# Kernel tuning notes

Measured on AMD Instinct MI355X. Metric: run time of the kernel, lower is better.

Reference implementation:

```python
import jax, jax.numpy as jnp
import numpy as np

NUM_EXPERTS = 32
TOP_K = 4
HIDDEN = 2048
INTER = 768


def setup_inputs() -> dict:
    key = jax.random.key(0)
    k1, k2, k3, k4 = jax.random.split(key, 4)
    hidden_states = jax.random.normal(k1, (4, 512, HIDDEN), dtype=jnp.float32)
    gate = jax.random.normal(k2, (HIDDEN, NUM_EXPERTS), dtype=jnp.float32) * 0.02
    gate_up_proj = jax.random.normal(k3, (NUM_EXPERTS, HIDDEN, 2 * INTER), dtype=jnp.float32) * 0.02
    down_proj = jax.random.normal(k4, (NUM_EXPERTS, INTER, HIDDEN), dtype=jnp.float32) * 0.02
    return {"hidden_states": hidden_states, "gate": gate,
            "gate_up_proj": gate_up_proj, "down_proj": down_proj}


def reference(hidden_states, gate, gate_up_proj, down_proj):
    batch_size = hidden_states.shape[0]
    x = hidden_states.reshape(-1, HIDDEN)  # (T, D)
    num_tokens = x.shape[0]

    # Router
    router_logits = jnp.einsum('TD,DE->TE', x, gate)
    routing_weights = jax.nn.softmax(router_logits.astype(jnp.float32), axis=-1)
    top_k_weights, top_k_indices = jax.lax.top_k(routing_weights, TOP_K)
    top_k_weights = top_k_weights / top_k_weights.sum(axis=-1, keepdims=True)
    top_k_weights = top_k_weights.astype(x.dtype)

    # Scatter top-k weights into full (T, E) matrix
    router_weights = jnp.zeros((num_tokens, NUM_EXPERTS), dtype=x.dtype)
    token_indices = jnp.broadcast_to(jnp.arange(num_tokens)[:, None], top_k_indices.shape)
    router_weights = router_weights.at[token_indices, top_k_indices].set(top_k_weights)

    # Dense all-expert experts pass (faithful to original: computes every expert per token)
    gate_up = jnp.einsum('TD,EDF->TEF', x, gate_up_proj)  # (T, E, 2F)
    g, u = jnp.split(gate_up, 2, axis=-1)
    gated = u * jax.nn.silu(g)  # (T, E, F)
    next_states = jnp.einsum('TEF,EFD->TED', gated, down_proj)
    next_states = (next_states * router_weights[..., None]).sum(axis=1)  # (T, D)
    return next_states.reshape(batch_size, -1, HIDDEN)
```

## Files before the change

kernel.cpp:

```cpp
#include <hip/hip_runtime.h>

#define T_TOKENS 2048
#define HIDDEN   2048
#define NEXPERT  32
#define TOPK     4
#define INTER    768
#define NPAIRS   (T_TOKENS*TOPK)
#define BM       128
#define BK       32
#define MT_MAX   95
#define NT1      12
#define NT2      16
#define NK1      (HIDDEN/BK)
#define NK2      (INTER/BK)

typedef short  bh8 __attribute__((ext_vector_type(8)));
typedef float  fx4 __attribute__((ext_vector_type(4)));

#define AS1 __attribute__((address_space(1)))
#define AS3 __attribute__((address_space(3)))

__device__ __forceinline__ void gload_lds16(const void* g, const void* lds_generic){
    __builtin_amdgcn_global_load_lds(
        (const AS1 void*)(unsigned long long)g,
        (AS3 void*)(unsigned int)(unsigned long long)lds_generic,
        16, 0, 0);
}

__device__ __forceinline__ unsigned int pack2bf(float a, float b){
    unsigned ua = __float_as_uint(a) + 0x8000u;
    unsigned ub = __float_as_uint(b) + 0x8000u;
    return __builtin_amdgcn_perm(ub, ua, 0x07060302u);
}
__device__ __forceinline__ unsigned short f2bfu(float f){
    return (unsigned short)((__float_as_uint(f) + 0x8000u) >> 16);
}

__global__ void cvt_x_k(const float* __restrict__ x, unsigned short* __restrict__ xb){
    int i = (blockIdx.x*256 + threadIdx.x)*8;
    float4 a = *(const float4*)(x+i);
    float4 b = *(const float4*)(x+i+4);
    uint4 o;
    o.x = pack2bf(a.x,a.y); o.y = pack2bf(a.z,a.w);
    o.z = pack2bf(b.x,b.y); o.w = pack2bf(b.z,b.w);
    *(uint4*)(xb+i) = o;
}

__global__ void router_k(const float* __restrict__ x, const float* __restrict__ gate,
                         int* __restrict__ topk_id, float* __restrict__ topk_w,
                         int* __restrict__ counts){
    const int t = blockIdx.x;
    const int l = threadIdx.x;
    const float* xr = x + (size_t)t*HIDDEN;
    float acc[NEXPERT];
#pragma unroll
    for (int e=0;e<NEXPERT;e++) acc[e]=0.f;
    for (int d=l; d<HIDDEN; d+=64){
        float xv = xr[d];
        const float4* g4 = (const float4*)(gate + (size_t)d*NEXPERT);
#pragma unroll
        for (int i=0;i<8;i++){
            float4 g = g4[i];
            acc[i*4+0] += xv*g.x; acc[i*4+1] += xv*g.y;
            acc[i*4+2] += xv*g.z; acc[i*4+3] += xv*g.w;
        }
    }
#pragma unroll
    for (int e=0;e<NEXPERT;e++){
#pragma unroll
        for (int m=1;m<64;m<<=1) acc[e] += __shfl_xor(acc[e], m, 64);
    }
    int ids[TOPK]; float lv[TOPK];
#pragma unroll
    for (int k=0;k<TOPK;k++){
        float m=-1e30f; int mi=0;
#pragma unroll
        for (int e=0;e<NEXPERT;e++){ if (acc[e]>m){ m=acc[e]; mi=e; } }
        ids[k]=mi; lv[k]=m; acc[mi]=-1e30f;
    }
    float ex[TOPK]; float s=0.f;
#pragma unroll
    for (int k=0;k<TOPK;k++){ ex[k]=__expf(lv[k]-lv[0]); s+=ex[k]; }
    if (l==0){
        float inv = 1.f/s;
#pragma unroll
        for (int k=0;k<TOPK;k++){
            topk_id[t*TOPK+k]=ids[k];
            topk_w[t*TOPK+k]=ex[k]*inv;
            atomicAdd(&counts[ids[k]],1);
        }
    }
}

__global__ void sched_k(const int* __restrict__ counts, int* __restrict__ offs,
                        int* __restrict__ cursors, int* __restrict__ nmt,
                        int* __restrict__ te, int* __restrict__ tr0, int* __restrict__ trn){
    if (threadIdx.x==0 && blockIdx.x==0){
        int tot=0, nm=0;
        for (int e=0;e<NEXPERT;e++){
            int c = counts[e];
            offs[e]=tot; cursors[e]=tot;
            for (int s=0;s<c;s+=BM){
                te[nm]=e; tr0[nm]=tot+s; trn[nm]=(c-s)<BM?(c-s):BM; nm++;
            }
            tot+=c;
        }
        *nmt = nm;
    }
}

__global__ void scatter_k(const int* __restrict__ topk_id, const float* __restrict__ topk_w,
                          int* __restrict__ cursors, int* __restrict__ pair_tok,
                          float* __restrict__ pair_w){
    int g = blockIdx.x*256 + threadIdx.x;
    int e = topk_id[g];
    float w = topk_w[g];
    int pos = atomicAdd(&cursors[e],1);
    pair_tok[pos] = g>>2;
    pair_w[pos]  = w;
}

__global__ __launch_bounds__(256) void gemm1_k(
        const unsigned short* __restrict__ xb, const float* __restrict__ gup,
        const int* __restrict__ nmt, const int* __restrict__ te,
        const int* __restrict__ tr0, const int* __restrict__ trn,
        const int* __restrict__ pair_tok, const float* __restrict__ pair_w,
        unsigned short* __restrict__ gated){
    __shared__ __align__(16) unsigned short As[2][BM*32];
    __shared__ __align__(16) unsigned short Bs[BM*40];
    __shared__ int   s_tok[BM];
    __shared__ float s_w[BM];

    const int nwg = gridDim.x;
    const int q = nwg>>3, r = nwg&7;
    const int xcd = blockIdx.x & 7, bidx = blockIdx.x >> 3;
    const int L = (xcd<r ? xcd*(q+1) : r*(q+1)+(xcd-r)*q) + bidx;
    const int mt = L % MT_MAX, nt = L / MT_MAX;
    if (mt >= *nmt) return;
    const int e = te[mt], row0 = tr0[mt], rows = trn[mt];
    const int n0 = nt*64;

    const int t = threadIdx.x;
    if (t < BM){
        int p = row0 + t; if (p > NPAIRS-1) p = NPAIRS-1;
        s_tok[t] = pair_tok[p];
        s_w[t]   = pair_w[p];
    }
    __syncthreads();

    const int w = t>>6, lane = t&63;
    const int l15 = lane & 15, kb = lane >> 4;

    const int arow0 = w*16 + (lane>>2);
    const int arow1 = 64 + arow0;
    const int ck0 = (lane&3) ^ ((lane>>3)&3);
    const unsigned short* asrc0 = xb + (size_t)s_tok[arow0]*HIDDEN + ck0*8;
    const unsigned short* asrc1 = xb + (size_t)s_tok[arow1]*HIDDEN + ck0*8;
    const unsigned short* adst0[2] = { &As[0][(w*16)*32],      &As[1][(w*16)*32] };
    const unsigned short* adst1[2] = { &As[0][(64+w*16)*32],   &As[1][(64+w*16)*32] };

    const int j5 = t & 31, col4 = j5*4;
    const int bd0 = (t>>5)*4;
    const int gq = (j5>>1)&3;
    const unsigned wb = (unsigned)(col4*80 + (((bd0>>3) ^ gq)<<4) + (bd0&4)*2);
    const int fc = (col4 < 64) ? (n0 + col4) : (704 + n0 + col4);
    const float* bsrc = gup + (size_t)e*HIDDEN*(2*INTER) + (size_t)bd0*(2*INTER) + fc;

    fx4 acc[2][8];
#pragma unroll
    for (int i=0;i<2;i++)
#pragma unroll
        for (int j=0;j<8;j++) acc[i][j] = (fx4)0.f;

    gload_lds16(asrc0, adst0[0]);
    gload_lds16(asrc1, adst1[0]);
    float4 rv0 = *(const float4*)(bsrc);
    float4 rv1 = *(const float4*)(bsrc + 2*INTER);
    float4 rv2 = *(const float4*)(bsrc + 4*INTER);
    float4 rv3 = *(const float4*)(bsrc + 6*INTER);

    const int sA = (l15>>1)&3;
    char* bsb = (char*)Bs;
    for (int k=0; k<NK1; ++k){
        __syncthreads();
        *(uint2*)(bsb + wb      ) = make_uint2(pack2bf(rv0.x,rv1.x), pack2bf(rv2.x,rv3.x));
        *(uint2*)(bsb + wb +  80) = make_uint2(pack2bf(rv0.y,rv1.y), pack2bf(rv2.y,rv3.y));
        *(uint2*)(bsb + wb + 160) = make_uint2(pack2bf(rv0.z,rv1.z), pack2bf(rv2.z,rv3.z));
        *(uint2*)(bsb + wb + 240) = make_uint2(pack2bf(rv0.w,rv1.w), pack2bf(rv2.w,rv3.w));
        __syncthreads();
        if (k+1 < NK1){
            const float* b2 = bsrc + (size_t)(k+1)*BK*(2*INTER);
            rv0 = *(const float4*)(b2);
            rv1 = *(const float4*)(b2 + 2*INTER);
            rv2 = *(const float4*)(b2 + 4*INTER);
            rv3 = *(const float4*)(b2 + 6*INTER);
            gload_lds16(asrc0 + (k+1)*BK, adst0[(k+1)&1]);
            gload_lds16(asrc1 + (k+1)*BK, adst1[(k+1)&1]);
        }
        const unsigned short* Ak = As[k&1];
        bh8 a0 = *(const bh8*)(Ak + (w*32+l15)*32    + ((kb ^ sA)<<3));
        bh8 a1 = *(const bh8*)(Ak + (w*32+16+l15)*32 + ((kb ^ sA)<<3));
#pragma unroll
        for (int c=0;c<8;c++){
            const int bc = c*16 + l15;
            bh8 b = *(const bh8*)(bsb + bc*80 + ((kb ^ ((bc>>3)&3))<<4));
            acc[0][c] = __builtin_amdgcn_mfma_f32_16x16x32_bf16(a0, b, acc[0][c], 0,0,0);
            acc[1][c] = __builtin_amdgcn_mfma_f32_16x16x32_bf16(a1, b, acc[1][c], 0,0,0);
        }
    }

    const int rbase = w*32 + kb*4;
#pragma unroll
    for (int mr=0;mr<2;mr++){
#pragma unroll
        for (int qq=0;qq<4;qq++){
            int row = rbase + mr*16 + qq;
            if (row < rows){
                float wgt = s_w[row];
                size_t prow = (size_t)(row0 + row)*INTER + n0 + l15;
#pragma unroll
                for (int c=0;c<4;c++){
                    float g = acc[mr][c][qq], u = acc[mr][c+4][qq];
                    float sil = g / (1.f + __expf(-g));
                    gated[prow + c*16] = f2bfu(sil*u*wgt);
                }
            }
        }
    }
}

__global__ __launch_bounds__(256) void gemm2_k(
        const unsigned short* __restrict__ gated, const float* __restrict__ down,
        const int* __restrict__ nmt, const int* __restrict__ te,
        const int* __restrict__ tr0, const int* __restrict__ trn,
        const int* __restrict__ pair_tok, float* __restrict__ out){
    __shared__ __align__(16) unsigned short As[2][BM*32];
    __shared__ __align__(16) unsigned short Bs[BM*40];
    __shared__ int s_tok[BM];

    const int nwg = gridDim.x;
    const int q = nwg>>3, r = nwg&7;
    const int xcd = blockIdx.x & 7, bidx = blockIdx.x >> 3;
    const int L = (xcd<r ? xcd*(q+1) : r*(q+1)+(xcd-r)*q) + bidx;
    const int mt = L % MT_MAX, nt = L / MT_MAX;
    if (mt >= *nmt) return;
    const int e = te[mt], row0 = tr0[mt], rows = trn[mt];
    const int n0 = nt*128;

    const int t = threadIdx.x;
    if (t < BM){
        int p = row0 + t; if (p > NPAIRS-1) p = NPAIRS-1;
        s_tok[t] = pair_tok[p];
    }
    __syncthreads();

    const int w = t>>6, lane = t&63;
    const int l15 = lane & 15, kb = lane >> 4;

    const int arow0 = w*16 + (lane>>2);
    const int arow1 = 64 + arow0;
    const int ck0 = (lane&3) ^ ((lane>>3)&3);
    const unsigned short* asrc0 = gated + (size_t)(row0 + arow0)*INTER + ck0*8;
    const unsigned short* asrc1 = gated + (size_t)(row0 + arow1)*INTER + ck0*8;
    const unsigned short* adst0[2] = { &As[0][(w*16)*32],    &As[1][(w*16)*32] };
    const unsigned short* adst1[2] = { &As[0][(64+w*16)*32], &As[1][(64+w*16)*32] };

    const int j5 = t & 31, col4 = j5*4;
    const int bd0 = (t>>5)*4;
    const int gq = (j5>>1)&3;
    const unsigned wb = (unsigned)(col4*80 + (((bd0>>3) ^ gq)<<4) + (bd0&4)*2);
    const float* bsrc = down + (size_t)e*INTER*HIDDEN + (size_t)bd0*HIDDEN + (n0 + col4);

    fx4 acc[2][8];
#pragma unroll
    for (int i=0;i<2;i++)
#pragma unroll
        for (int j=0;j<8;j++) acc[i][j] = (fx4)0.f;

    gload_lds16(asrc0, adst0[0]);
    gload_lds16(asrc1, adst1[0]);
    float4 rv0 = *(const float4*)(bsrc);
    float4 rv1 = *(const float4*)(bsrc + HIDDEN);
    float4 rv2 = *(const float4*)(bsrc + 2*HIDDEN);
    float4 rv3 = *(const float4*)(bsrc + 3*HIDDEN);

    const int sA = (l15>>1)&3;
    char* bsb = (char*)Bs;
    for (int k=0; k<NK2; ++k){
        __syncthreads();
        *(uint2*)(bsb + wb      ) = make_uint2(pack2bf(rv0.x,rv1.x), pack2bf(rv2.x,rv3.x));
        *(uint2*)(bsb + wb +  80) = make_uint2(pack2bf(rv0.y,rv1.y), pack2bf(rv2.y,rv3.y));
        *(uint2*)(bsb + wb + 160) = make_uint2(pack2bf(rv0.z,rv1.z), pack2bf(rv2.z,rv3.z));
        *(uint2*)(bsb + wb + 240) = make_uint2(pack2bf(rv0.w,rv1.w), pack2bf(rv2.w,rv3.w));
        __syncthreads();
        if (k+1 < NK2){
            const float* b2 = bsrc + (size_t)(k+1)*BK*HIDDEN;
            rv0 = *(const float4*)(b2);
            rv1 = *(const float4*)(b2 + HIDDEN);
            rv2 = *(const float4*)(b2 + 2*HIDDEN);
            rv3 = *(const float4*)(b2 + 3*HIDDEN);
            gload_lds16(asrc0 + (k+1)*BK, adst0[(k+1)&1]);
            gload_lds16(asrc1 + (k+1)*BK, adst1[(k+1)&1]);
        }
        const unsigned short* Ak = As[k&1];
        bh8 a0 = *(const bh8*)(Ak + (w*32+l15)*32    + ((kb ^ sA)<<3));
        bh8 a1 = *(const bh8*)(Ak + (w*32+16+l15)*32 + ((kb ^ sA)<<3));
#pragma unroll
        for (int c=0;c<8;c++){
            const int bc = c*16 + l15;
            bh8 b = *(const bh8*)(bsb + bc*80 + ((kb ^ ((bc>>3)&3))<<4));
            acc[0][c] = __builtin_amdgcn_mfma_f32_16x16x32_bf16(a0, b, acc[0][c], 0,0,0);
            acc[1][c] = __builtin_amdgcn_mfma_f32_16x16x32_bf16(a1, b, acc[1][c], 0,0,0);
        }
    }

    const int rbase = w*32 + kb*4;
#pragma unroll
    for (int mr=0;mr<2;mr++){
#pragma unroll
        for (int qq=0;qq<4;qq++){
            int row = rbase + mr*16 + qq;
            if (row < rows){
                float* orow = out + (size_t)s_tok[row]*HIDDEN + n0 + l15;
#pragma unroll
                for (int c=0;c<8;c++)
                    atomicAdd(orow + c*16, acc[mr][c][qq]);
            }
        }
    }
}

extern "C" void kernel_launch(void* const* d_in, const int* in_sizes, int n_in,
                              void* d_out, int out_size, void* d_ws, size_t ws_size,
                              hipStream_t stream){
    const float* x    = (const float*)d_in[0];
    const float* gate = (const float*)d_in[1];
    const float* gup  = (const float*)d_in[2];
    const float* down = (const float*)d_in[3];
    float* out = (float*)d_out;
    char*  ws  = (char*)d_ws;

    int*   topk_id  = (int*)  (ws + 0x00000);
    float* topk_w   = (float*)(ws + 0x08000);
    int*   counts   = (int*)  (ws + 0x10000);
    int*   cursors  = (int*)  (ws + 0x10080);
    int*   offs     = (int*)  (ws + 0x10100);
    int*   nmt      = (int*)  (ws + 0x10180);
    int*   te       = (int*)  (ws + 0x10200);
    int*   tr0      = (int*)  (ws + 0x10400);
    int*   trn      = (int*)  (ws + 0x10600);
    int*   pair_tok = (int*)  (ws + 0x10800);
    float* pair_w   = (float*)(ws + 0x18800);
    unsigned short* gated = (unsigned short*)(ws + 0x21000);
    unsigned short* xb    = (unsigned short*)(ws + 0xC60000);

    hipMemsetAsync(d_out, 0, (size_t)out_size*sizeof(float), stream);
    hipMemsetAsync(counts, 0, NEXPERT*sizeof(int), stream);

    cvt_x_k  <<<T_TOKENS*HIDDEN/(256*8), 256, 0, stream>>>(x, xb);
    router_k <<<T_TOKENS, 64, 0, stream>>>(x, gate, topk_id, topk_w, counts);
    sched_k  <<<1, 64, 0, stream>>>(counts, offs, cursors, nmt, te, tr0, trn);
    scatter_k<<<NPAIRS/256, 256, 0, stream>>>(topk_id, topk_w, cursors, pair_tok, pair_w);
    gemm1_k  <<<MT_MAX*NT1, 256, 0, stream>>>(xb, gup, nmt, te, tr0, trn, pair_tok, pair_w, gated);
    gemm2_k  <<<MT_MAX*NT2, 256, 0, stream>>>(gated, down, nmt, te, tr0, trn, pair_tok, out);
}
```

Baseline: 429.0 us.

## Halve GEMM N-tiles and double-buffer B tile with single barrier per k-step

```diff
diff --git a/kernel.cpp b/kernel.cpp
--- a/kernel.cpp
+++ b/kernel.cpp
@@ -9,8 +9,8 @@
 #define BM       128
 #define BK       32
 #define MT_MAX   95
-#define NT1      12
-#define NT2      16
+#define NT1      24
+#define NT2      32
 #define NK1      (HIDDEN/BK)
 #define NK2      (INTER/BK)
 
@@ -120,6 +120,15 @@
     pair_w[pos]  = w;
 }
 
+#define TILE_DECODE(NT)                                            \
+    const int nwg = gridDim.x;                                     \
+    const int q = nwg>>3, r = nwg&7;                               \
+    const int xcd = blockIdx.x & 7, bidx = blockIdx.x >> 3;        \
+    const int L = (xcd<r ? xcd*(q+1) : r*(q+1)+(xcd-r)*q) + bidx;  \
+    const int mt = L % MT_MAX, nt = L / MT_MAX;                    \
+    if (mt >= *nmt) return;                                        \
+    const int e = te[mt], row0 = tr0[mt], rows = trn[mt];
+
 __global__ __launch_bounds__(256) void gemm1_k(
         const unsigned short* __restrict__ xb, const float* __restrict__ gup,
         const int* __restrict__ nmt, const int* __restrict__ te,
@@ -127,18 +136,12 @@
         const int* __restrict__ pair_tok, const float* __restrict__ pair_w,
         unsigned short* __restrict__ gated){
     __shared__ __align__(16) unsigned short As[2][BM*32];
-    __shared__ __align__(16) unsigned short Bs[BM*40];
+    __shared__ __align__(16) unsigned short Bs[2][64*40];
     __shared__ int   s_tok[BM];
     __shared__ float s_w[BM];
 
-    const int nwg = gridDim.x;
-    const int q = nwg>>3, r = nwg&7;
-    const int xcd = blockIdx.x & 7, bidx = blockIdx.x >> 3;
-    const int L = (xcd<r ? xcd*(q+1) : r*(q+1)+(xcd-r)*q) + bidx;
-    const int mt = L % MT_MAX, nt = L / MT_MAX;
-    if (mt >= *nmt) return;
-    const int e = te[mt], row0 = tr0[mt], rows = trn[mt];
-    const int n0 = nt*64;
+    TILE_DECODE(NT1)
+    const int n0 = nt*32;
 
     const int t = threadIdx.x;
     if (t < BM){
@@ -150,64 +153,77 @@
 
     const int w = t>>6, lane = t&63;
     const int l15 = lane & 15, kb = lane >> 4;
+    const int sA = (l15>>1)&3;
 
     const int arow0 = w*16 + (lane>>2);
     const int arow1 = 64 + arow0;
     const int ck0 = (lane&3) ^ ((lane>>3)&3);
     const unsigned short* asrc0 = xb + (size_t)s_tok[arow0]*HIDDEN + ck0*8;
     const unsigned short* asrc1 = xb + (size_t)s_tok[arow1]*HIDDEN + ck0*8;
-    const unsigned short* adst0[2] = { &As[0][(w*16)*32],      &As[1][(w*16)*32] };
-    const unsigned short* adst1[2] = { &As[0][(64+w*16)*32],   &As[1][(64+w*16)*32] };
-
-    const int j5 = t & 31, col4 = j5*4;
-    const int bd0 = (t>>5)*4;
-    const int gq = (j5>>1)&3;
-    const unsigned wb = (unsigned)(col4*80 + (((bd0>>3) ^ gq)<<4) + (bd0&4)*2);
-    const int fc = (col4 < 64) ? (n0 + col4) : (704 + n0 + col4);
+
+    const int col4 = (t&15)*4;
+    const int bd0  = (t>>4)*2;
+    const int sB   = (col4>>3)&3;
+    const unsigned wb = (unsigned)(col4*80 + (((bd0>>3) ^ sB)<<4) + (bd0&7)*2);
+    const int fc = (col4 < 32) ? (n0 + col4) : (736 + n0 + col4);
     const float* bsrc = gup + (size_t)e*HIDDEN*(2*INTER) + (size_t)bd0*(2*INTER) + fc;
 
-    fx4 acc[2][8];
+    fx4 acc[2][4];
 #pragma unroll
     for (int i=0;i<2;i++)
 #pragma unroll
-        for (int j=0;j<8;j++) acc[i][j] = (fx4)0.f;
-
-    gload_lds16(asrc0, adst0[0]);
-    gload_lds16(asrc1, adst1[0]);
+        for (int j=0;j<4;j++) acc[i][j] = (fx4)0.f;
+
     float4 rv0 = *(const float4*)(bsrc);
     float4 rv1 = *(const float4*)(bsrc + 2*INTER);
-    float4 rv2 = *(const float4*)(bsrc + 4*INTER);
-    float4 rv3 = *(const float4*)(bsrc + 6*INTER);
-
-    const int sA = (l15>>1)&3;
-    char* bsb = (char*)Bs;
-    for (int k=0; k<NK1; ++k){
-        __syncthreads();
-        *(uint2*)(bsb + wb      ) = make_uint2(pack2bf(rv0.x,rv1.x), pack2bf(rv2.x,rv3.x));
-        *(uint2*)(bsb + wb +  80) = make_uint2(pack2bf(rv0.y,rv1.y), pack2bf(rv2.y,rv3.y));
-        *(uint2*)(bsb + wb + 160) = make_uint2(pack2bf(rv0.z,rv1.z), pack2bf(rv2.z,rv3.z));
-        *(uint2*)(bsb + wb + 240) = make_uint2(pack2bf(rv0.w,rv1.w), pack2bf(rv2.w,rv3.w));
-        __syncthreads();
-        if (k+1 < NK1){
-            const float* b2 = bsrc + (size_t)(k+1)*BK*(2*INTER);
-            rv0 = *(const float4*)(b2);
-            rv1 = *(const float4*)(b2 + 2*INTER);
-            rv2 = *(const float4*)(b2 + 4*INTER);
-            rv3 = *(const float4*)(b2 + 6*INTER);
-            gload_lds16(asrc0 + (k+1)*BK, adst0[(k+1)&1]);
-            gload_lds16(asrc1 + (k+1)*BK, adst1[(k+1)&1]);
-        }
-        const unsigned short* Ak = As[k&1];
-        bh8 a0 = *(const bh8*)(Ak + (w*32+l15)*32    + ((kb ^ sA)<<3));
-        bh8 a1 = *(const bh8*)(Ak + (w*32+16+l15)*32 + ((kb ^ sA)<<3));
-#pragma unroll
-        for (int c=0;c<8;c++){
-            const int bc = c*16 + l15;
-            bh8 b = *(const bh8*)(bsb + bc*80 + ((kb ^ ((bc>>3)&3))<<4));
-            acc[0][c] = __builtin_amdgcn_mfma_f32_16x16x32_bf16(a0, b, acc[0][c], 0,0,0);
-            acc[1][c] = __builtin_amdgcn_mfma_f32_16x16x32_bf16(a1, b, acc[1][c], 0,0,0);
-        }
-    }
+    gload_lds16(asrc0, &As[0][(w*16)*32]);
+    gload_lds16(asrc1, &As[0][(64+w*16)*32]);
+    __syncthreads();
+    {
+        char* bw = (char*)Bs[0];
+        *(unsigned*)(bw + wb      ) = pack2bf(rv0.x, rv1.x);
+        *(unsigned*)(bw + wb +  80) = pack2bf(rv0.y, rv1.y);
+        *(unsigned*)(bw + wb + 160) = pack2bf(rv0.z, rv1.z);
+        *(unsigned*)(bw + wb + 240) = pack2bf(rv0.w, rv1.w);
+    }
+    __syncthreads();
+
+#define G1_STEP(KK, CUR, NXT) do{                                              \
+    const int _kn = (KK)+1;                                                    \
+    if (_kn < NK1){                                                            \
+        const float* _b2 = bsrc + (size_t)_kn*BK*(2*INTER);                    \
+        rv0 = *(const float4*)(_b2);                                           \
+        rv1 = *(const float4*)(_b2 + 2*INTER);                                 \
+        gload_lds16(asrc0 + _kn*BK, &As[NXT][(w*16)*32]);                      \
+        gload_lds16(asrc1 + _kn*BK, &As[NXT][(64+w*16)*32]);                   \
+    }                                                                          \
+    {   const unsigned short* _Ak = As[CUR];                                   \
+        const char* _Bk = (const char*)Bs[CUR];                                \
+        bh8 _a0 = *(const bh8*)(_Ak + (w*32+l15)*32    + ((kb ^ sA)<<3));      \
+        bh8 _a1 = *(const bh8*)(_Ak + (w*32+16+l15)*32 + ((kb ^ sA)<<3));      \
+        _Pragma("unroll")                                                      \
+        for (int c=0;c<4;c++){                                                 \
+            const int bc = c*16 + l15;                                         \
+            bh8 _b = *(const bh8*)(_Bk + bc*80 + ((kb ^ ((bc>>3)&3))<<4));     \
+            acc[0][c] = __builtin_amdgcn_mfma_f32_16x16x32_bf16(_a0,_b,acc[0][c],0,0,0); \
+            acc[1][c] = __builtin_amdgcn_mfma_f32_16x16x32_bf16(_a1,_b,acc[1][c],0,0,0); \
+        }                                                                      \
+    }                                                                          \
+    if (_kn < NK1){                                                            \
+        char* _bw = (char*)Bs[NXT];                                            \
+        *(unsigned*)(_bw + wb      ) = pack2bf(rv0.x, rv1.x);                  \
+        *(unsigned*)(_bw + wb +  80) = pack2bf(rv0.y, rv1.y);                  \
+        *(unsigned*)(_bw + wb + 160) = pack2bf(rv0.z, rv1.z);                  \
+        *(unsigned*)(_bw + wb + 240) = pack2bf(rv0.w, rv1.w);                  \
+    }                                                                          \
+    __syncthreads();                                                           \
+}while(0)
+
+    for (int k2=0; k2<NK1; k2+=2){
+        G1_STEP(k2,   0, 1);
+        G1_STEP(k2+1, 1, 0);
+    }
+#undef G1_STEP
 
     const int rbase = w*32 + kb*4;
 #pragma unroll
@@ -219,8 +235,8 @@
                 float wgt = s_w[row];
                 size_t prow = (size_t)(row0 + row)*INTER + n0 + l15;
 #pragma unroll
-                for (int c=0;c<4;c++){
-                    float g = acc[mr][c][qq], u = acc[mr][c+4][qq];
+                for (int c=0;c<2;c++){
+                    float g = acc[mr][c][qq], u = acc[mr][c+2][qq];
                     float sil = g / (1.f + __expf(-g));
                     gated[prow + c*16] = f2bfu(sil*u*wgt);
                 }
@@ -235,17 +251,11 @@
         const int* __restrict__ tr0, const int* __restrict__ trn,
         const int* __restrict__ pair_tok, float* __restrict__ out){
     __shared__ __align__(16) unsigned short As[2][BM*32];
-    __shared__ __align__(16) unsigned short Bs[BM*40];
+    __shared__ __align__(16) unsigned short Bs[2][64*40];
     __shared__ int s_tok[BM];
 
-    const int nwg = gridDim.x;
-    const int q = nwg>>3, r = nwg&7;
-    const int xcd = blockIdx.x & 7, bidx = blockIdx.x >> 3;
-    const int L = (xcd<r ? xcd*(q+1) : r*(q+1)+(xcd-r)*q) + bidx;
-    const int mt = L % MT_MAX, nt = L / MT_MAX;
-    if (mt >= *nmt) return;
-    const int e = te[mt], row0 = tr0[mt], rows = trn[mt];
-    const int n0 = nt*128;
+    TILE_DECODE(NT2)
+    const int n0 = nt*64;
 
     const int t = threadIdx.x;
     if (t < BM){
@@ -256,63 +266,78 @@
 
     const int w = t>>6, lane = t&63;
     const int l15 = lane & 15, kb = lane >> 4;
+    const int sA = (l15>>1)&3;
 
     const int arow0 = w*16 + (lane>>2);
     const int arow1 = 64 + arow0;
     const int ck0 = (lane&3) ^ ((lane>>3)&3);
-    const unsigned short* asrc0 = gated + (size_t)(row0 + arow0)*INTER + ck0*8;
-    const unsigned short* asrc1 = gated + (size_t)(row0 + arow1)*INTER + ck0*8;
-    const unsigned short* adst0[2] = { &As[0][(w*16)*32],    &As[1][(w*16)*32] };
-    const unsigned short* adst1[2] = { &As[0][(64+w*16)*32], &As[1][(64+w*16)*32] };
-
-    const int j5 = t & 31, col4 = j5*4;
-    const int bd0 = (t>>5)*4;
-    const int gq = (j5>>1)&3;
-    const unsigned wb = (unsigned)(col4*80 + (((bd0>>3) ^ gq)<<4) + (bd0&4)*2);
+    int ap0 = row0 + arow0; if (ap0 > NPAIRS-1) ap0 = NPAIRS-1;
+    int ap1 = row0 + arow1; if (ap1 > NPAIRS-1) ap1 = NPAIRS-1;
+    const unsigned short* asrc0 = gated + (size_t)ap0*INTER + ck0*8;
+    const unsigned short* asrc1 = gated + (size_t)ap1*INTER + ck0*8;
+
+    const int col4 = (t&15)*4;
+    const int bd0  = (t>>4)*2;
+    const int sB   = (col4>>3)&3;
+    const unsigned wb = (unsigned)(col4*80 + (((bd0>>3) ^ sB)<<4) + (bd0&7)*2);
     const float* bsrc = down + (size_t)e*INTER*HIDDEN + (size_t)bd0*HIDDEN + (n0 + col4);
 
-    fx4 acc[2][8];
+    fx4 acc[2][4];
 #pragma unroll
     for (int i=0;i<2;i++)
 #pragma unroll
-        for (int j=0;j<8;j++) acc[i][j] = (fx4)0.f;
-
-    gload_lds16(asrc0, adst0[0]);
-    gload_lds16(asrc1, adst1[0]);
+        for (int j=0;j<4;j++) acc[i][j] = (fx4)0.f;
+
     float4 rv0 = *(const float4*)(bsrc);
     float4 rv1 = *(const float4*)(bsrc + HIDDEN);
-    float4 rv2 = *(const float4*)(bsrc + 2*HIDDEN);
-    float4 rv3 = *(const float4*)(bsrc + 3*HIDDEN);
-
-    const int sA = (l15>>1)&3;
-    char* bsb = (char*)Bs;
-    for (int k=0; k<NK2; ++k){
-        __syncthreads();
-        *(uint2*)(bsb + wb      ) = make_uint2(pack2bf(rv0.x,rv1.x), pack2bf(rv2.x,rv3.x));
-        *(uint2*)(bsb + wb +  80) = make_uint2(pack2bf(rv0.y,rv1.y), pack2bf(rv2.y,rv3.y));
-        *(uint2*)(bsb + wb + 160) = make_uint2(pack2bf(rv0.z,rv1.z), pack2bf(rv2.z,rv3.z));
-        *(uint2*)(bsb + wb + 240) = make_uint2(pack2bf(rv0.w,rv1.w), pack2bf(rv2.w,rv3.w));
-        __syncthreads();
-        if (k+1 < NK2){
-            const float* b2 = bsrc + (size_t)(k+1)*BK*HIDDEN;
-            rv0 = *(const float4*)(b2);
-            rv1 = *(const float4*)(b2 + HIDDEN);
-            rv2 = *(const float4*)(b2 + 2*HIDDEN);
-            rv3 = *(const float4*)(b2 + 3*HIDDEN);
-            gload_lds16(asrc0 + (k+1)*BK, adst0[(k+1)&1]);
-            gload_lds16(asrc1 + (k+1)*BK, adst1[(k+1)&1]);
-        }
-        const unsigned short* Ak = As[k&1];
-        bh8 a0 = *(const bh8*)(Ak + (w*32+l15)*32    + ((kb ^ sA)<<3));
-        bh8 a1 = *(const bh8*)(Ak + (w*32+16+l15)*32 + ((kb ^ sA)<<3));
-#pragma unroll
-        for (int c=0;c<8;c++){
-            const int bc = c*16 + l15;
-            bh8 b = *(const bh8*)(bsb + bc*80 + ((kb ^ ((bc>>3)&3))<<4));
-            acc[0][c] = __builtin_amdgcn_mfma_f32_16x16x32_bf16(a0, b, acc[0][c], 0,0,0);
-            acc[1][c] = __builtin_amdgcn_mfma_f32_16x16x32_bf16(a1, b, acc[1][c], 0,0,0);
-        }
-    }
+    gload_lds16(asrc0, &As[0][(w*16)*32]);
+    gload_lds16(asrc1, &As[0][(64+w*16)*32]);
+    __syncthreads();
+    {
+        char* bw = (char*)Bs[0];
+        *(unsigned*)(bw + wb      ) = pack2bf(rv0.x, rv1.x);
+        *(unsigned*)(bw + wb +  80) = pack2bf(rv0.y, rv1.y);
+        *(unsigned*)(bw + wb + 160) = pack2bf(rv0.z, rv1.z);
+        *(unsigned*)(bw + wb + 240) = pack2bf(rv0.w, rv1.w);
+    }
+    __syncthreads();
+
+#define G2_STEP(KK, CUR, NXT) do{                                              \
+    const int _kn = (KK)+1;                                                    \
+    if (_kn < NK2){                                                            \
+        const float* _b2 = bsrc + (size_t)_kn*BK*HIDDEN;                       \
+        rv0 = *(const float4*)(_b2);                                           \
+        rv1 = *(const float4*)(_b2 + HIDDEN);                                  \
+        gload_lds16(asrc0 + _kn*BK, &As[NXT][(w*16)*32]);                      \
+        gload_lds16(asrc1 + _kn*BK, &As[NXT][(64+w*16)*32]);                   \
+    }                                                                          \
+    {   const unsigned short* _Ak = As[CUR];                                   \
+        const char* _Bk = (const char*)Bs[CUR];                                \
+        bh8 _a0 = *(const bh8*)(_Ak + (w*32+l15)*32    + ((kb ^ sA)<<3));      \
+        bh8 _a1 = *(const bh8*)(_Ak + (w*32+16+l15)*32 + ((kb ^ sA)<<3));      \
+        _Pragma("unroll")                                                      \
+        for (int c=0;c<4;c++){                                                 \
+            const int bc = c*16 + l15;                                         \
+            bh8 _b = *(const bh8*)(_Bk + bc*80 + ((kb ^ ((bc>>3)&3))<<4));     \
+            acc[0][c] = __builtin_amdgcn_mfma_f32_16x16x32_bf16(_a0,_b,acc[0][c],0,0,0); \
+            acc[1][c] = __builtin_amdgcn_mfma_f32_16x16x32_bf16(_a1,_b,acc[1][c],0,0,0); \
+        }                                                                      \
+    }                                                                          \
+    if (_kn < NK2){                                                            \
+        char* _bw = (char*)Bs[NXT];                                            \
+        *(unsigned*)(_bw + wb      ) = pack2bf(rv0.x, rv1.x);                  \
+        *(unsigned*)(_bw + wb +  80) = pack2bf(rv0.y, rv1.y);                  \
+        *(unsigned*)(_bw + wb + 160) = pack2bf(rv0.z, rv1.z);                  \
+        *(unsigned*)(_bw + wb + 240) = pack2bf(rv0.w, rv1.w);                  \
+    }                                                                          \
+    __syncthreads();                                                           \
+}while(0)
+
+    for (int k2=0; k2<NK2; k2+=2){
+        G2_STEP(k2,   0, 1);
+        G2_STEP(k2+1, 1, 0);
+    }
+#undef G2_STEP
 
     const int rbase = w*32 + kb*4;
 #pragma unroll
@@ -323,7 +348,7 @@
             if (row < rows){
                 float* orow = out + (size_t)s_tok[row]*HIDDEN + n0 + l15;
 #pragma unroll
-                for (int c=0;c<8;c++)
+                for (int c=0;c<4;c++)
                     atomicAdd(orow + c*16, acc[mr][c][qq]);
             }
         }
```

Result: slower. 471.6 us (+9.9%).

## Widen GEMM N-tiles to 256 with 512-thread blocks and double-buffered B

Applied to the files above, without the earlier changes.

```diff
diff --git a/kernel.cpp b/kernel.cpp
--- a/kernel.cpp
+++ b/kernel.cpp
@@ -5,12 +5,13 @@
 #define NEXPERT  32
 #define TOPK     4
 #define INTER    768
+#define GUF      (2*INTER)
 #define NPAIRS   (T_TOKENS*TOPK)
 #define BM       128
 #define BK       32
 #define MT_MAX   95
-#define NT1      12
-#define NT2      16
+#define NT1      6
+#define NT2      8
 #define NK1      (HIDDEN/BK)
 #define NK2      (INTER/BK)
 
@@ -34,6 +35,9 @@
 }
 __device__ __forceinline__ unsigned short f2bfu(float f){
     return (unsigned short)((__float_as_uint(f) + 0x8000u) >> 16);
+}
+__device__ __forceinline__ float bf2f(unsigned short s){
+    return __uint_as_float(((unsigned)s)<<16);
 }
 
 __global__ void cvt_x_k(const float* __restrict__ x, unsigned short* __restrict__ xb){
@@ -120,51 +124,47 @@
     pair_w[pos]  = w;
 }
 
-__global__ __launch_bounds__(256) void gemm1_k(
+#define TILE_DECODE()                                              \
+    const int nwg = gridDim.x;                                     \
+    const int q = nwg>>3, r = nwg&7;                               \
+    const int xcd = blockIdx.x & 7, bidx = blockIdx.x >> 3;        \
+    const int L = (xcd<r ? xcd*(q+1) : r*(q+1)+(xcd-r)*q) + bidx;  \
+    const int mt = L % MT_MAX, nt = L / MT_MAX;                    \
+    if (mt >= *nmt) return;                                        \
+    const int e = te[mt], row0 = tr0[mt], rows = trn[mt];
+
+__global__ __launch_bounds__(512,4) void gemm1_k(
         const unsigned short* __restrict__ xb, const float* __restrict__ gup,
         const int* __restrict__ nmt, const int* __restrict__ te,
         const int* __restrict__ tr0, const int* __restrict__ trn,
-        const int* __restrict__ pair_tok, const float* __restrict__ pair_w,
-        unsigned short* __restrict__ gated){
+        const int* __restrict__ pair_tok,
+        unsigned short* __restrict__ gu){
     __shared__ __align__(16) unsigned short As[2][BM*32];
-    __shared__ __align__(16) unsigned short Bs[BM*40];
-    __shared__ int   s_tok[BM];
-    __shared__ float s_w[BM];
-
-    const int nwg = gridDim.x;
-    const int q = nwg>>3, r = nwg&7;
-    const int xcd = blockIdx.x & 7, bidx = blockIdx.x >> 3;
-    const int L = (xcd<r ? xcd*(q+1) : r*(q+1)+(xcd-r)*q) + bidx;
-    const int mt = L % MT_MAX, nt = L / MT_MAX;
-    if (mt >= *nmt) return;
-    const int e = te[mt], row0 = tr0[mt], rows = trn[mt];
-    const int n0 = nt*64;
+    __shared__ __align__(16) unsigned short Bs[2][256*40];
+    __shared__ int s_tok[BM];
+
+    TILE_DECODE()
+    const int n0 = nt*256;
 
     const int t = threadIdx.x;
     if (t < BM){
         int p = row0 + t; if (p > NPAIRS-1) p = NPAIRS-1;
         s_tok[t] = pair_tok[p];
-        s_w[t]   = pair_w[p];
     }
     __syncthreads();
 
     const int w = t>>6, lane = t&63;
     const int l15 = lane & 15, kb = lane >> 4;
-
-    const int arow0 = w*16 + (lane>>2);
-    const int arow1 = 64 + arow0;
+    const int wr = w & 3, wc = w >> 2;
+    const int sA = (l15>>1)&3;
+
+    const int arow = w*16 + (lane>>2);
     const int ck0 = (lane&3) ^ ((lane>>3)&3);
-    const unsigned short* asrc0 = xb + (size_t)s_tok[arow0]*HIDDEN + ck0*8;
-    const unsigned short* asrc1 = xb + (size_t)s_tok[arow1]*HIDDEN + ck0*8;
-    const unsigned short* adst0[2] = { &As[0][(w*16)*32],      &As[1][(w*16)*32] };
-    const unsigned short* adst1[2] = { &As[0][(64+w*16)*32],   &As[1][(64+w*16)*32] };
-
-    const int j5 = t & 31, col4 = j5*4;
-    const int bd0 = (t>>5)*4;
-    const int gq = (j5>>1)&3;
-    const unsigned wb = (unsigned)(col4*80 + (((bd0>>3) ^ gq)<<4) + (bd0&4)*2);
-    const int fc = (col4 < 64) ? (n0 + col4) : (704 + n0 + col4);
-    const float* bsrc = gup + (size_t)e*HIDDEN*(2*INTER) + (size_t)bd0*(2*INTER) + fc;
+    const unsigned short* asrc = xb + (size_t)s_tok[arow]*HIDDEN + ck0*8;
+
+    const int cp = t & 127, kh = t >> 7;
+    const float* bsrc = gup + (size_t)e*HIDDEN*GUF + (size_t)kh*8*GUF + (n0 + 2*cp);
+    const unsigned wb0 = (unsigned)((2*cp)*80 + ((kh ^ (cp&3))<<4));
 
     fx4 acc[2][8];
 #pragma unroll
@@ -172,80 +172,100 @@
 #pragma unroll
         for (int j=0;j<8;j++) acc[i][j] = (fx4)0.f;
 
-    gload_lds16(asrc0, adst0[0]);
-    gload_lds16(asrc1, adst1[0]);
-    float4 rv0 = *(const float4*)(bsrc);
-    float4 rv1 = *(const float4*)(bsrc + 2*INTER);
-    float4 rv2 = *(const float4*)(bsrc + 4*INTER);
-    float4 rv3 = *(const float4*)(bsrc + 6*INTER);
-
-    const int sA = (l15>>1)&3;
-    char* bsb = (char*)Bs;
-    for (int k=0; k<NK1; ++k){
+    float2 f0,f1,f2,f3,f4,f5,f6,f7;
+
+#define LOADB1(KS) do{ const float* _bp = bsrc + (size_t)(KS)*BK*GUF;           \
+    f0=*(const float2*)(_bp);        f1=*(const float2*)(_bp+GUF);              \
+    f2=*(const float2*)(_bp+2*GUF);  f3=*(const float2*)(_bp+3*GUF);            \
+    f4=*(const float2*)(_bp+4*GUF);  f5=*(const float2*)(_bp+5*GUF);            \
+    f6=*(const float2*)(_bp+6*GUF);  f7=*(const float2*)(_bp+7*GUF); }while(0)
+
+#define WRITEB(BUF) do{ char* _bb = (char*)Bs[BUF];                             \
+    uint4 _c0, _c1;                                                             \
+    _c0.x=pack2bf(f0.x,f1.x); _c0.y=pack2bf(f2.x,f3.x);                         \
+    _c0.z=pack2bf(f4.x,f5.x); _c0.w=pack2bf(f6.x,f7.x);                         \
+    _c1.x=pack2bf(f0.y,f1.y); _c1.y=pack2bf(f2.y,f3.y);                         \
+    _c1.z=pack2bf(f4.y,f5.y); _c1.w=pack2bf(f6.y,f7.y);                         \
+    *(uint4*)(_bb + wb0) = _c0; *(uint4*)(_bb + wb0 + 80) = _c1; }while(0)
+
+#define STAGEA1(KS,BUF) gload_lds16(asrc + (KS)*BK, &As[BUF][(w*16)*32])
+
+#define COMPUTE(BUF) do{                                                        \
+    const unsigned short* _Ak = As[BUF];                                        \
+    const char* _Bb = (const char*)Bs[BUF];                                     \
+    bh8 _a0 = *(const bh8*)(_Ak + (wr*32+l15)*32    + ((kb^sA)<<3));            \
+    bh8 _a1 = *(const bh8*)(_Ak + (wr*32+16+l15)*32 + ((kb^sA)<<3));            \
+    _Pragma("unroll")                                                           \
+    for (int c=0;c<8;c++){                                                      \
+        bh8 _b = *(const bh8*)(_Bb + (wc*128 + c*16 + l15)*80 + ((kb^sA)<<4));  \
+        acc[0][c] = __builtin_amdgcn_mfma_f32_16x16x32_bf16(_a0,_b,acc[0][c],0,0,0); \
+        acc[1][c] = __builtin_amdgcn_mfma_f32_16x16x32_bf16(_a1,_b,acc[1][c],0,0,0); \
+    } }while(0)
+
+    STAGEA1(0,0); LOADB1(0);
+    __syncthreads();
+    WRITEB(0);
+    __syncthreads();
+
+    for (int k=0;k<NK1;k++){
+        const int kn = k+1;
+        if (kn < NK1){ LOADB1(kn); STAGEA1(kn, kn&1); }
+        COMPUTE(k&1);
         __syncthreads();
-        *(uint2*)(bsb + wb      ) = make_uint2(pack2bf(rv0.x,rv1.x), pack2bf(rv2.x,rv3.x));
-        *(uint2*)(bsb + wb +  80) = make_uint2(pack2bf(rv0.y,rv1.y), pack2bf(rv2.y,rv3.y));
-        *(uint2*)(bsb + wb + 160) = make_uint2(pack2bf(rv0.z,rv1.z), pack2bf(rv2.z,rv3.z));
-        *(uint2*)(bsb + wb + 240) = make_uint2(pack2bf(rv0.w,rv1.w), pack2bf(rv2.w,rv3.w));
+        if (kn < NK1) WRITEB(kn&1);
         __syncthreads();
-        if (k+1 < NK1){
-            const float* b2 = bsrc + (size_t)(k+1)*BK*(2*INTER);
-            rv0 = *(const float4*)(b2);
-            rv1 = *(const float4*)(b2 + 2*INTER);
-            rv2 = *(const float4*)(b2 + 4*INTER);
-            rv3 = *(const float4*)(b2 + 6*INTER);
-            gload_lds16(asrc0 + (k+1)*BK, adst0[(k+1)&1]);
-            gload_lds16(asrc1 + (k+1)*BK, adst1[(k+1)&1]);
-        }
-        const unsigned short* Ak = As[k&1];
-        bh8 a0 = *(const bh8*)(Ak + (w*32+l15)*32    + ((kb ^ sA)<<3));
-        bh8 a1 = *(const bh8*)(Ak + (w*32+16+l15)*32 + ((kb ^ sA)<<3));
-#pragma unroll
-        for (int c=0;c<8;c++){
-            const int bc = c*16 + l15;
-            bh8 b = *(const bh8*)(bsb + bc*80 + ((kb ^ ((bc>>3)&3))<<4));
-            acc[0][c] = __builtin_amdgcn_mfma_f32_16x16x32_bf16(a0, b, acc[0][c], 0,0,0);
-            acc[1][c] = __builtin_amdgcn_mfma_f32_16x16x32_bf16(a1, b, acc[1][c], 0,0,0);
-        }
-    }
-
-    const int rbase = w*32 + kb*4;
+    }
+
+    const int rbase = wr*32 + kb*4;
 #pragma unroll
     for (int mr=0;mr<2;mr++){
 #pragma unroll
         for (int qq=0;qq<4;qq++){
             int row = rbase + mr*16 + qq;
             if (row < rows){
-                float wgt = s_w[row];
-                size_t prow = (size_t)(row0 + row)*INTER + n0 + l15;
-#pragma unroll
-                for (int c=0;c<4;c++){
-                    float g = acc[mr][c][qq], u = acc[mr][c+4][qq];
-                    float sil = g / (1.f + __expf(-g));
-                    gated[prow + c*16] = f2bfu(sil*u*wgt);
-                }
+                size_t prow = (size_t)(row0 + row)*GUF + n0 + wc*128 + l15;
+#pragma unroll
+                for (int c=0;c<8;c++)
+                    gu[prow + c*16] = f2bfu(acc[mr][c][qq]);
             }
         }
     }
-}
-
-__global__ __launch_bounds__(256) void gemm2_k(
+#undef LOADB1
+#undef STAGEA1
+}
+
+__global__ void silu_k(const unsigned short* __restrict__ gu,
+                       const float* __restrict__ pair_w,
+                       unsigned short* __restrict__ gated){
+    const int t = threadIdx.x;
+    const int r = (t >= 96) ? 1 : 0;
+    const int jg = t - r*96;
+    const int p = blockIdx.x*2 + r;
+    bh8 g8 = *(const bh8*)(gu + (size_t)p*GUF + jg*8);
+    bh8 u8 = *(const bh8*)(gu + (size_t)p*GUF + INTER + jg*8);
+    float wgt = pair_w[p];
+    bh8 o;
+#pragma unroll
+    for (int j=0;j<8;j++){
+        float g = bf2f((unsigned short)g8[j]);
+        float u = bf2f((unsigned short)u8[j]);
+        float sil = g / (1.f + __expf(-g));
+        o[j] = (short)f2bfu(sil*u*wgt);
+    }
+    *(bh8*)(gated + (size_t)p*INTER + jg*8) = o;
+}
+
+__global__ __launch_bounds__(512,4) void gemm2_k(
         const unsigned short* __restrict__ gated, const float* __restrict__ down,
         const int* __restrict__ nmt, const int* __restrict__ te,
         const int* __restrict__ tr0, const int* __restrict__ trn,
         const int* __restrict__ pair_tok, float* __restrict__ out){
     __shared__ __align__(16) unsigned short As[2][BM*32];
-    __shared__ __align__(16) unsigned short Bs[BM*40];
+    __shared__ __align__(16) unsigned short Bs[2][256*40];
     __shared__ int s_tok[BM];
 
-    const int nwg = gridDim.x;
-    const int q = nwg>>3, r = nwg&7;
-    const int xcd = blockIdx.x & 7, bidx = blockIdx.x >> 3;
-    const int L = (xcd<r ? xcd*(q+1) : r*(q+1)+(xcd-r)*q) + bidx;
-    const int mt = L % MT_MAX, nt = L / MT_MAX;
-    if (mt >= *nmt) return;
-    const int e = te[mt], row0 = tr0[mt], rows = trn[mt];
-    const int n0 = nt*128;
+    TILE_DECODE()
+    const int n0 = nt*256;
 
     const int t = threadIdx.x;
     if (t < BM){
@@ -256,20 +276,17 @@
 
     const int w = t>>6, lane = t&63;
     const int l15 = lane & 15, kb = lane >> 4;
-
-    const int arow0 = w*16 + (lane>>2);
-    const int arow1 = 64 + arow0;
+    const int wr = w & 3, wc = w >> 2;
+    const int sA = (l15>>1)&3;
+
+    const int arow = w*16 + (lane>>2);
     const int ck0 = (lane&3) ^ ((lane>>3)&3);
-    const unsigned short* asrc0 = gated + (size_t)(row0 + arow0)*INTER + ck0*8;
-    const unsigned short* asrc1 = gated + (size_t)(row0 + arow1)*INTER + ck0*8;
-    const unsigned short* adst0[2] = { &As[0][(w*16)*32],    &As[1][(w*16)*32] };
-    const unsigned short* adst1[2] = { &As[0][(64+w*16)*32], &As[1][(64+w*16)*32] };
-
-    const int j5 = t & 31, col4 = j5*4;
-    const int bd0 = (t>>5)*4;
-    const int gq = (j5>>1)&3;
-    const unsigned wb = (unsigned)(col4*80 + (((bd0>>3) ^ gq)<<4) + (bd0&4)*2);
-    const float* bsrc = down + (size_t)e*INTER*HIDDEN + (size_t)bd0*HIDDEN + (n0 + col4);
+    int ap = row0 + arow; if (ap > NPAIRS-1) ap = NPAIRS-1;
+    const unsigned short* asrc = gated + (size_t)ap*INTER + ck0*8;
+
+    const int cp = t & 127, kh = t >> 7;
+    const float* bsrc = down + (size_t)e*INTER*HIDDEN + (size_t)kh*8*HIDDEN + (n0 + 2*cp);
+    const unsigned wb0 = (unsigned)((2*cp)*80 + ((kh ^ (cp&3))<<4));
 
     fx4 acc[2][8];
 #pragma unroll
@@ -277,51 +294,38 @@
 #pragma unroll
         for (int j=0;j<8;j++) acc[i][j] = (fx4)0.f;
 
-    gload_lds16(asrc0, adst0[0]);
-    gload_lds16(asrc1, adst1[0]);
-    float4 rv0 = *(const float4*)(bsrc);
-    float4 rv1 = *(const float4*)(bsrc + HIDDEN);
-    float4 rv2 = *(const float4*)(bsrc + 2*HIDDEN);
-    float4 rv3 = *(const float4*)(bsrc + 3*HIDDEN);
-
-    const int sA = (l15>>1)&3;
-    char* bsb = (char*)Bs;
-    for (int k=0; k<NK2; ++k){
+    float2 f0,f1,f2,f3,f4,f5,f6,f7;
+
+#define LOADB2(KS) do{ const float* _bp = bsrc + (size_t)(KS)*BK*HIDDEN;        \
+    f0=*(const float2*)(_bp);           f1=*(const float2*)(_bp+HIDDEN);        \
+    f2=*(const float2*)(_bp+2*HIDDEN);  f3=*(const float2*)(_bp+3*HIDDEN);      \
+    f4=*(const float2*)(_bp+4*HIDDEN);  f5=*(const float2*)(_bp+5*HIDDEN);      \
+    f6=*(const float2*)(_bp+6*HIDDEN);  f7=*(const float2*)(_bp+7*HIDDEN); }while(0)
+
+#define STAGEA2(KS,BUF) gload_lds16(asrc + (KS)*BK, &As[BUF][(w*16)*32])
+
+    STAGEA2(0,0); LOADB2(0);
+    __syncthreads();
+    WRITEB(0);
+    __syncthreads();
+
+    for (int k=0;k<NK2;k++){
+        const int kn = k+1;
+        if (kn < NK2){ LOADB2(kn); STAGEA2(kn, kn&1); }
+        COMPUTE(k&1);
         __syncthreads();
-        *(uint2*)(bsb + wb      ) = make_uint2(pack2bf(rv0.x,rv1.x), pack2bf(rv2.x,rv3.x));
-        *(uint2*)(bsb + wb +  80) = make_uint2(pack2bf(rv0.y,rv1.y), pack2bf(rv2.y,rv3.y));
-        *(uint2*)(bsb + wb + 160) = make_uint2(pack2bf(rv0.z,rv1.z), pack2bf(rv2.z,rv3.z));
-        *(uint2*)(bsb + wb + 240) = make_uint2(pack2bf(rv0.w,rv1.w), pack2bf(rv2.w,rv3.w));
+        if (kn < NK2) WRITEB(kn&1);
         __syncthreads();
-        if (k+1 < NK2){
-            const float* b2 = bsrc + (size_t)(k+1)*BK*HIDDEN;
-            rv0 = *(const float4*)(b2);
-            rv1 = *(const float4*)(b2 + HIDDEN);
-            rv2 = *(const float4*)(b2 + 2*HIDDEN);
-            rv3 = *(const float4*)(b2 + 3*HIDDEN);
-            gload_lds16(asrc0 + (k+1)*BK, adst0[(k+1)&1]);
-            gload_lds16(asrc1 + (k+1)*BK, adst1[(k+1)&1]);
-        }
-        const unsigned short* Ak = As[k&1];
-        bh8 a0 = *(const bh8*)(Ak + (w*32+l15)*32    + ((kb ^ sA)<<3));
-        bh8 a1 = *(const bh8*)(Ak + (w*32+16+l15)*32 + ((kb ^ sA)<<3));
-#pragma unroll
-        for (int c=0;c<8;c++){
-            const int bc = c*16 + l15;
-            bh8 b = *(const bh8*)(bsb + bc*80 + ((kb ^ ((bc>>3)&3))<<4));
-            acc[0][c] = __builtin_amdgcn_mfma_f32_16x16x32_bf16(a0, b, acc[0][c], 0,0,0);
-            acc[1][c] = __builtin_amdgcn_mfma_f32_16x16x32_bf16(a1, b, acc[1][c], 0,0,0);
-        }
-    }
-
-    const int rbase = w*32 + kb*4;
+    }
+
+    const int rbase = wr*32 + kb*4;
 #pragma unroll
     for (int mr=0;mr<2;mr++){
 #pragma unroll
         for (int qq=0;qq<4;qq++){
             int row = rbase + mr*16 + qq;
             if (row < rows){
-                float* orow = out + (size_t)s_tok[row]*HIDDEN + n0 + l15;
+                float* orow = out + (size_t)s_tok[row]*HIDDEN + n0 + wc*128 + l15;
 #pragma unroll
                 for (int c=0;c<8;c++)
                     atomicAdd(orow + c*16, acc[mr][c][qq]);
@@ -353,6 +357,7 @@
     float* pair_w   = (float*)(ws + 0x18800);
     unsigned short* gated = (unsigned short*)(ws + 0x21000);
     unsigned short* xb    = (unsigned short*)(ws + 0xC60000);
+    unsigned short* gu    = (unsigned short*)(ws + 0x1460000);
 
     hipMemsetAsync(d_out, 0, (size_t)out_size*sizeof(float), stream);
     hipMemsetAsync(counts, 0, NEXPERT*sizeof(int), stream);
@@ -361,6 +366,7 @@
     router_k <<<T_TOKENS, 64, 0, stream>>>(x, gate, topk_id, topk_w, counts);
     sched_k  <<<1, 64, 0, stream>>>(counts, offs, cursors, nmt, te, tr0, trn);
     scatter_k<<<NPAIRS/256, 256, 0, stream>>>(topk_id, topk_w, cursors, pair_tok, pair_w);
-    gemm1_k  <<<MT_MAX*NT1, 256, 0, stream>>>(xb, gup, nmt, te, tr0, trn, pair_tok, pair_w, gated);
-    gemm2_k  <<<MT_MAX*NT2, 256, 0, stream>>>(gated, down, nmt, te, tr0, trn, pair_tok, out);
-}
+    gemm1_k  <<<MT_MAX*NT1, 512, 0, stream>>>(xb, gup, nmt, te, tr0, trn, pair_tok, gu);
+    silu_k   <<<NPAIRS/2, 192, 0, stream>>>(gu, pair_w, gated);
+    gemm2_k  <<<MT_MAX*NT2, 512, 0, stream>>>(gated, down, nmt, te, tr0, trn, pair_tok, out);
+}
```

Measured after the change: 510.9 us. 19.1% more time.
